# Kernel tuning notes

Hardware: AMD Instinct MI355X
Metric: run time of the kernel (lower is better)

## Reference

```python
import jax, jax.numpy as jnp
import numpy as np

B, S, N, E = 4, 256, 257, 256  # batch, seq_len, num_nodes (=S+1), num_edges (=S)
IN, OUT, EDIM = 128, 128, 16


def setup_inputs() -> dict:
    key = jax.random.key(0)
    k = jax.random.split(key, 7)
    x = jax.random.normal(k[0], (B, S, N, IN), jnp.float32)
    ei = jax.random.randint(k[1], (B, S, E, 2), 0, N)
    drop = jax.random.uniform(k[2], (B, S, E, 2)) < 0.05
    edge_index = jnp.where(drop, -1, ei)
    edge_attr = jax.random.normal(k[3], (B, S, E, EDIM), jnp.float32)
    node_mask = jnp.ones((B, S, N), dtype=bool)  # accepted but unused by forward
    edge_mask = jax.random.uniform(k[4], (B, S, E)) > 0.1
    W = jax.random.normal(k[5], (IN, OUT), jnp.float32) * (1.0 / np.sqrt(IN))
    a = jax.random.normal(k[6], (2 * OUT + EDIM, 1), jnp.float32) * 0.05
    return {"x": x, "edge_index": edge_index, "edge_attr": edge_attr,
            "node_mask": node_mask, "edge_mask": edge_mask, "W": W, "a": a}


def reference(x, edge_index, edge_attr, node_mask, edge_mask, W, a):
    # x: [B,S,N,IN] -> h: [B,S,N,D]
    h = x @ W
    Bq, Sq = h.shape[0], h.shape[1]
    src_idx = edge_index[..., 0]  # [B,S,E]
    tgt_idx = edge_index[..., 1]

    def gather(idx):  # [B,S,E] -> [B,S,E,D], gather node features along node dim
        return jnp.take_along_axis(h, jnp.clip(idx, 0, None)[..., None], axis=2)

    # src/tgt features, zeroed where index < 0 (invalid edge endpoint)
    src = jnp.where((src_idx >= 0)[..., None], gather(src_idx), 0.0)
    tgt = jnp.where((tgt_idx >= 0)[..., None], gather(tgt_idx), 0.0)

    # attention logits over concatenated [src | tgt | edge_attr]
    cat = jnp.concatenate([src, tgt, edge_attr], axis=-1)  # [B,S,E,2D+edim]
    e = jax.nn.leaky_relu((cat @ a)[..., 0], negative_slope=0.2)  # [B,S,E]
    e = jnp.where(edge_mask, e, -jnp.inf)
    # rows with no finite entry are zeroed (-> uniform softmax), as in torch code
    all_invalid = ~jnp.isfinite(e).any(axis=-1, keepdims=True)
    e = jnp.where(all_invalid, 0.0, e)
    alpha = jax.nn.softmax(e, axis=-1)  # [B,S,E]

    # masked edges get index 0 (they still contribute alpha-weighted feats to node 0,
    # matching the original scatter semantics)
    vsrc = jnp.where(edge_mask, src_idx, 0)
    vtgt = jnp.where(edge_mask, tgt_idx, 0)
    x_src = jnp.take_along_axis(h, vsrc[..., None], axis=2) * alpha[..., None]
    x_tgt = jnp.take_along_axis(h, vtgt[..., None], axis=2) * alpha[..., None]

    # scatter-add over edges into node buffer (equivalent to the torch 5D
    # scatter_ + sum over the edge dim, without materializing [B,S,E,N,D])
    bi = jnp.arange(Bq)[:, None, None]
    si = jnp.arange(Sq)[None, :, None]
    agg = (jnp.zeros(h.shape, h.dtype)
           .at[bi, si, vtgt].add(x_src)
           .at[bi, si, vsrc].add(x_tgt))
    return jax.nn.elu(agg)
```

## Files before the change

### kernel.cpp

```cpp
#include <hip/hip_runtime.h>
#include <cfloat>
#include <cmath>


#define BB 4
#define SS 256
#define NNODE 257
#define EE 256
#define DIN 128
#define DOUT 128
#define EDIMC 16
#define NMASK (BB * SS * EE)

#define WS_FLAG_OFF  0
#define WS_MASK_OFF  1024
#define WS_ALPHA_OFF 266240

__global__ void detect_mask_kernel(const unsigned int* __restrict__ m, int* flag) {
    unsigned int v = 0;
    for (int i = threadIdx.x; i < 256; i += 64) v |= m[i];
    int bad = (v > 1u) ? 1 : 0;
    bad = __any(bad) ? 1 : 0;
    if (threadIdx.x == 0) *flag = bad;
}

__global__ __launch_bounds__(256) void mask_canon_kernel(
        const int* __restrict__ m32, const unsigned char* __restrict__ m8,
        const int* __restrict__ flag, unsigned char* __restrict__ out) {
    const bool byteLayout = (*flag != 0);
    int i = blockIdx.x * 256 + threadIdx.x;
    if (i < NMASK) out[i] = byteLayout ? (m8[i] != 0) : (m32[i] != 0);
}

__global__ __launch_bounds__(256) void gemm_kernel(const float* __restrict__ x,
                                                   const float* __restrict__ W,
                                                   float* __restrict__ h) {
    __shared__ float xs[32][132];
    __shared__ float wsh[32][132];
    const int tid = threadIdx.x;
    const long m0 = (long)blockIdx.x * 128;
    const int tm = tid >> 4;
    const int tn = tid & 15;
    const int mr = tm * 8, nr = tn * 8;
    float acc[8][8];
#pragma unroll
    for (int i = 0; i < 8; ++i)
#pragma unroll
        for (int j = 0; j < 8; ++j) acc[i][j] = 0.f;

    for (int kt = 0; kt < 4; ++kt) {
#pragma unroll
        for (int j = 0; j < 4; ++j) {
            int idx = j * 256 + tid;
            int row = idx >> 3;
            int kq  = idx & 7;
            float4 v = *reinterpret_cast<const float4*>(
                x + (m0 + row) * DIN + kt * 32 + kq * 4);
            xs[kq * 4 + 0][row] = v.x;
            xs[kq * 4 + 1][row] = v.y;
            xs[kq * 4 + 2][row] = v.z;
            xs[kq * 4 + 3][row] = v.w;
        }
#pragma unroll
        for (int j = 0; j < 4; ++j) {
            int idx = j * 256 + tid;
            int row = idx >> 5;
            int nq  = idx & 31;
            float4 v = *reinterpret_cast<const float4*>(
                W + (kt * 32 + row) * DOUT + nq * 4);
            *reinterpret_cast<float4*>(&wsh[row][nq * 4]) = v;
        }
        __syncthreads();
#pragma unroll
        for (int k = 0; k < 32; ++k) {
            float4 a0 = *reinterpret_cast<const float4*>(&xs[k][mr]);
            float4 a1 = *reinterpret_cast<const float4*>(&xs[k][mr + 4]);
            float4 b0 = *reinterpret_cast<const float4*>(&wsh[k][nr]);
            float4 b1 = *reinterpret_cast<const float4*>(&wsh[k][nr + 4]);
            float av[8] = {a0.x, a0.y, a0.z, a0.w, a1.x, a1.y, a1.z, a1.w};
            float bv[8] = {b0.x, b0.y, b0.z, b0.w, b1.x, b1.y, b1.z, b1.w};
#pragma unroll
            for (int i = 0; i < 8; ++i)
#pragma unroll
                for (int jj = 0; jj < 8; ++jj)
                    acc[i][jj] = fmaf(av[i], bv[jj], acc[i][jj]);
        }
        __syncthreads();
    }
#pragma unroll
    for (int i = 0; i < 8; ++i) {
        float* dst = h + (m0 + mr + i) * DOUT + nr;
        *reinterpret_cast<float4*>(dst) =
            make_float4(acc[i][0], acc[i][1], acc[i][2], acc[i][3]);
        *reinterpret_cast<float4*>(dst + 4) =
            make_float4(acc[i][4], acc[i][5], acc[i][6], acc[i][7]);
    }
}

__global__ __launch_bounds__(256) void alpha_kernel(
        const float* __restrict__ h, const int* __restrict__ eidx,
        const float* __restrict__ eattr, const unsigned char* __restrict__ emask,
        const float* __restrict__ a, float* __restrict__ alpha_out) {
    __shared__ float pq[NNODE], pt[NNODE];
    __shared__ float ae[EDIMC];
    __shared__ float red[4];
    __shared__ int redi[4];
    const int tid = threadIdx.x;
    const int bs = blockIdx.x;
    const int lane = tid & 63, wave = tid >> 6;
    if (tid < EDIMC) ae[tid] = a[2 * DOUT + tid];
    const float a0 = a[lane], a1 = a[lane + 64];
    const float a2 = a[128 + lane], a3 = a[192 + lane];
    const float* hb = h + (long)bs * NNODE * DIN;
    for (int n = wave; n < NNODE; n += 4) {
        const float* hr = hb + n * DIN;
        float v0 = hr[lane], v1 = hr[lane + 64];
        float s = v0 * a0 + v1 * a1;
        float t = v0 * a2 + v1 * a3;
#pragma unroll
        for (int o = 32; o > 0; o >>= 1) {
            s += __shfl_xor(s, o);
            t += __shfl_xor(t, o);
        }
        if (lane == 0) { pq[n] = s; pt[n] = t; }
    }
    __syncthreads();

    const int e = tid;
    const long ebase = (long)bs * EE + e;
    const int si = eidx[2 * ebase];
    const int ti = eidx[2 * ebase + 1];
    const float4* ea4 = reinterpret_cast<const float4*>(eattr + ebase * EDIMC);
    float dea = 0.f;
#pragma unroll
    for (int j = 0; j < 4; ++j) {
        float4 u = ea4[j];
        dea += u.x * ae[4 * j] + u.y * ae[4 * j + 1] +
               u.z * ae[4 * j + 2] + u.w * ae[4 * j + 3];
    }
    float val = (si >= 0 ? pq[si] : 0.f) + (ti >= 0 ? pt[ti] : 0.f) + dea;
    val = val > 0.f ? val : 0.2f * val;
    const bool m = emask[ebase] != 0;

    float lg = m ? val : -FLT_MAX;
    float wm = lg;
    int anyv = m ? 1 : 0;
#pragma unroll
    for (int o = 32; o > 0; o >>= 1) {
        wm = fmaxf(wm, __shfl_xor(wm, o));
        anyv |= __shfl_xor(anyv, o);
    }
    if (lane == 0) { red[wave] = wm; redi[wave] = anyv; }
    __syncthreads();
    const float gmax = fmaxf(fmaxf(red[0], red[1]), fmaxf(red[2], red[3]));
    const int ganyv = redi[0] | redi[1] | redi[2] | redi[3];
    float ex = m ? expf(val - gmax) : 0.f;
    float sm = ex;
#pragma unroll
    for (int o = 32; o > 0; o >>= 1) sm += __shfl_xor(sm, o);
    __syncthreads();
    if (lane == 0) red[wave] = sm;
    __syncthreads();
    const float gsum = red[0] + red[1] + red[2] + red[3];
    alpha_out[ebase] = ganyv ? ex / gsum : (1.0f / EE);
}

__global__ __launch_bounds__(256) void agg_kernel(
        const float* __restrict__ h, const int* __restrict__ eidx,
        const unsigned char* __restrict__ emask, const float* __restrict__ alpha,
        float* __restrict__ out) {
    __shared__ float agg[NNODE * 32];
    const int tid = threadIdx.x;
    const int bs = blockIdx.x;
    const int dbase = blockIdx.y * 32;
    const int slot = tid >> 5, d = tid & 31;
    for (int i = tid; i < NNODE * 32; i += 256) agg[i] = 0.f;
    __syncthreads();

    const float* hb = h + (long)bs * NNODE * DIN + dbase;
    const long eb0 = (long)bs * EE;
    for (int e0 = 0; e0 < EE; e0 += 8) {
        const int e = e0 + slot;
        const float al = alpha[eb0 + e];
        if (al != 0.f) {
            const int si = eidx[2 * (eb0 + e)];
            const int ti = eidx[2 * (eb0 + e) + 1];
            const bool m = emask[eb0 + e] != 0;
            int vs = m ? si : 0; if (vs < 0) vs += NNODE;
            int vt = m ? ti : 0; if (vt < 0) vt += NNODE;
            const float hs = hb[(long)vs * DIN + d];
            const float ht = hb[(long)vt * DIN + d];
            atomicAdd(&agg[vt * 32 + d], al * hs);
            atomicAdd(&agg[vs * 32 + d], al * ht);
        }
    }
    __syncthreads();

    float* ob = out + (long)bs * NNODE * DIN + dbase;
    for (int n = slot; n < NNODE; n += 8) {
        const float v = agg[n * 32 + d];
        ob[(long)n * DIN + d] = v > 0.f ? v : expm1f(v);
    }
}

extern "C" void kernel_launch(void* const* d_in, const int* in_sizes, int n_in,
                              void* d_out, int out_size, void* d_ws, size_t ws_size,
                              hipStream_t stream) {
    const float* x     = (const float*)d_in[0];
    const int* eidx    = (const int*)d_in[1];
    const float* eattr = (const float*)d_in[2];
    const void* emraw  = d_in[4];
    const float* W     = (const float*)d_in[5];
    const float* a     = (const float*)d_in[6];
    float* out = (float*)d_out;

    char* ws = (char*)d_ws;
    int* flag            = (int*)(ws + WS_FLAG_OFF);
    unsigned char* mask8 = (unsigned char*)(ws + WS_MASK_OFF);
    float* alpha         = (float*)(ws + WS_ALPHA_OFF);
    float* h             = out;

    detect_mask_kernel<<<1, 64, 0, stream>>>((const unsigned int*)emraw, flag);
    mask_canon_kernel<<<NMASK / 256, 256, 0, stream>>>(
        (const int*)emraw, (const unsigned char*)emraw, flag, mask8);

    const int M_BLOCKS = (BB * SS * NNODE) / 128;
    gemm_kernel<<<M_BLOCKS, 256, 0, stream>>>(x, W, h);
    alpha_kernel<<<BB * SS, 256, 0, stream>>>(h, eidx, eattr, mask8, a, alpha);
    agg_kernel<<<dim3(BB * SS, 4), 256, 0, stream>>>(h, eidx, mask8, alpha, out);
}
```

Before: 647.4 us.

## Fuse attention projections into GEMM epilogue and stage h slices in LDS for aggregation

The GEMM epilogue now computes the per-node dot products with the src and tgt halves of the attention vector, reducing across the 16 column threads with shuffles and writing pq/pt to workspace. A lighter alpha kernel then reads only those scalars instead of re-reading all of h. The aggregation kernel now splits the feature dimension into 16-wide slices, stages each slice of h and the edge metadata in shared memory, and accumulates with padded LDS atomics. This removes a full re-read of h and the scattered global gathers. In exchange it launches twice as many agg blocks, uses more LDS per block, and needs a larger workspace, falling back to the old path when the workspace is too small.

```diff
diff --git a/kernel.cpp b/kernel.cpp
--- a/kernel.cpp
+++ b/kernel.cpp
@@ -11,10 +11,14 @@
 #define DOUT 128
 #define EDIMC 16
 #define NMASK (BB * SS * EE)
+#define MROWS (BB * SS * NNODE)
 
 #define WS_FLAG_OFF  0
 #define WS_MASK_OFF  1024
 #define WS_ALPHA_OFF 266240
+#define WS_PQ_OFF    (WS_ALPHA_OFF + NMASK * 4)
+#define WS_PT_OFF    (WS_PQ_OFF + MROWS * 4)
+#define WS_NEEDED    (WS_PT_OFF + MROWS * 4)
 
 __global__ void detect_mask_kernel(const unsigned int* __restrict__ m, int* flag) {
     unsigned int v = 0;
@@ -34,7 +38,10 @@
 
 __global__ __launch_bounds__(256) void gemm_kernel(const float* __restrict__ x,
                                                    const float* __restrict__ W,
-                                                   float* __restrict__ h) {
+                                                   const float* __restrict__ a,
+                                                   float* __restrict__ h,
+                                                   float* __restrict__ pq,
+                                                   float* __restrict__ pt) {
     __shared__ float xs[32][132];
     __shared__ float wsh[32][132];
     const int tid = threadIdx.x;
@@ -95,6 +102,86 @@
         *reinterpret_cast<float4*>(dst + 4) =
             make_float4(acc[i][4], acc[i][5], acc[i][6], acc[i][7]);
     }
+
+    if (pq != nullptr) {
+        float aq[8], at_[8];
+#pragma unroll
+        for (int j = 0; j < 8; ++j) {
+            aq[j]  = a[nr + j];
+            at_[j] = a[DOUT + nr + j];
+        }
+#pragma unroll
+        for (int i = 0; i < 8; ++i) {
+            float s = 0.f, t = 0.f;
+#pragma unroll
+            for (int j = 0; j < 8; ++j) {
+                s = fmaf(acc[i][j], aq[j], s);
+                t = fmaf(acc[i][j], at_[j], t);
+            }
+#pragma unroll
+            for (int o = 1; o < 16; o <<= 1) {
+                s += __shfl_xor(s, o);
+                t += __shfl_xor(t, o);
+            }
+            if (tn == 0) {
+                pq[m0 + mr + i] = s;
+                pt[m0 + mr + i] = t;
+            }
+        }
+    }
+}
+
+__global__ __launch_bounds__(256) void alpha2_kernel(
+        const float* __restrict__ pq, const float* __restrict__ pt,
+        const int* __restrict__ eidx, const float* __restrict__ eattr,
+        const unsigned char* __restrict__ emask, const float* __restrict__ a,
+        float* __restrict__ alpha_out) {
+    __shared__ float ae[EDIMC];
+    __shared__ float red[4];
+    __shared__ int redi[4];
+    const int tid = threadIdx.x;
+    const int bs = blockIdx.x;
+    const int lane = tid & 63, wave = tid >> 6;
+    if (tid < EDIMC) ae[tid] = a[2 * DOUT + tid];
+    __syncthreads();
+
+    const long ebase = (long)bs * EE + tid;
+    const int si = eidx[2 * ebase];
+    const int ti = eidx[2 * ebase + 1];
+    const float4* ea4 = reinterpret_cast<const float4*>(eattr + ebase * EDIMC);
+    float dea = 0.f;
+#pragma unroll
+    for (int j = 0; j < 4; ++j) {
+        float4 u = ea4[j];
+        dea += u.x * ae[4 * j] + u.y * ae[4 * j + 1] +
+               u.z * ae[4 * j + 2] + u.w * ae[4 * j + 3];
+    }
+    const long nb = (long)bs * NNODE;
+    float val = (si >= 0 ? pq[nb + si] : 0.f) + (ti >= 0 ? pt[nb + ti] : 0.f) + dea;
+    val = val > 0.f ? val : 0.2f * val;
+    const bool m = emask[ebase] != 0;
+
+    float lg = m ? val : -FLT_MAX;
+    float wm = lg;
+    int anyv = m ? 1 : 0;
+#pragma unroll
+    for (int o = 32; o > 0; o >>= 1) {
+        wm = fmaxf(wm, __shfl_xor(wm, o));
+        anyv |= __shfl_xor(anyv, o);
+    }
+    if (lane == 0) { red[wave] = wm; redi[wave] = anyv; }
+    __syncthreads();
+    const float gmax = fmaxf(fmaxf(red[0], red[1]), fmaxf(red[2], red[3]));
+    const int ganyv = redi[0] | redi[1] | redi[2] | redi[3];
+    float ex = m ? expf(val - gmax) : 0.f;
+    float sm = ex;
+#pragma unroll
+    for (int o = 32; o > 0; o >>= 1) sm += __shfl_xor(sm, o);
+    __syncthreads();
+    if (lane == 0) red[wave] = sm;
+    __syncthreads();
+    const float gsum = red[0] + red[1] + red[2] + red[3];
+    alpha_out[ebase] = ganyv ? ex / gsum : (1.0f / EE);
 }
 
 __global__ __launch_bounds__(256) void alpha_kernel(
@@ -126,8 +213,7 @@
     }
     __syncthreads();
 
-    const int e = tid;
-    const long ebase = (long)bs * EE + e;
+    const long ebase = (long)bs * EE + tid;
     const int si = eidx[2 * ebase];
     const int ti = eidx[2 * ebase + 1];
     const float4* ea4 = reinterpret_cast<const float4*>(eattr + ebase * EDIMC);
@@ -165,40 +251,60 @@
     alpha_out[ebase] = ganyv ? ex / gsum : (1.0f / EE);
 }
 
+#define DSL 16
+#define PAD 17
 __global__ __launch_bounds__(256) void agg_kernel(
         const float* __restrict__ h, const int* __restrict__ eidx,
         const unsigned char* __restrict__ emask, const float* __restrict__ alpha,
         float* __restrict__ out) {
-    __shared__ float agg[NNODE * 32];
+    __shared__ float hs[NNODE * PAD];
+    __shared__ float acc[NNODE * PAD];
+    __shared__ float meta_a[EE];
+    __shared__ int   meta_v[EE];
     const int tid = threadIdx.x;
     const int bs = blockIdx.x;
-    const int dbase = blockIdx.y * 32;
-    const int slot = tid >> 5, d = tid & 31;
-    for (int i = tid; i < NNODE * 32; i += 256) agg[i] = 0.f;
-    __syncthreads();
+    const int dbase = blockIdx.y * DSL;
+    const int slot = tid >> 4, d = tid & 15;
 
     const float* hb = h + (long)bs * NNODE * DIN + dbase;
-    const long eb0 = (long)bs * EE;
-    for (int e0 = 0; e0 < EE; e0 += 8) {
+
+    for (int i = tid; i < NNODE * 4; i += 256) {
+        int row = i >> 2, q = i & 3;
+        float4 v = *reinterpret_cast<const float4*>(hb + (long)row * DIN + q * 4);
+        float* dst = &hs[row * PAD + q * 4];
+        dst[0] = v.x; dst[1] = v.y; dst[2] = v.z; dst[3] = v.w;
+    }
+    for (int i = tid; i < NNODE * PAD; i += 256) acc[i] = 0.f;
+    {
+        const long eb = (long)bs * EE + tid;
+        const int si = eidx[2 * eb];
+        const int ti = eidx[2 * eb + 1];
+        const bool m = emask[eb] != 0;
+        int vs = m ? si : 0; if (vs < 0) vs += NNODE;
+        int vt = m ? ti : 0; if (vt < 0) vt += NNODE;
+        meta_a[tid] = alpha[eb];
+        meta_v[tid] = vs | (vt << 16);
+    }
+    __syncthreads();
+
+#pragma unroll 4
+    for (int e0 = 0; e0 < EE; e0 += 16) {
         const int e = e0 + slot;
-        const float al = alpha[eb0 + e];
+        const float al = meta_a[e];
         if (al != 0.f) {
-            const int si = eidx[2 * (eb0 + e)];
-            const int ti = eidx[2 * (eb0 + e) + 1];
-            const bool m = emask[eb0 + e] != 0;
-            int vs = m ? si : 0; if (vs < 0) vs += NNODE;
-            int vt = m ? ti : 0; if (vt < 0) vt += NNODE;
-            const float hs = hb[(long)vs * DIN + d];
-            const float ht = hb[(long)vt * DIN + d];
-            atomicAdd(&agg[vt * 32 + d], al * hs);
-            atomicAdd(&agg[vs * 32 + d], al * ht);
+            const int pv = meta_v[e];
+            const int vs = pv & 0xffff, vt = pv >> 16;
+            const float hsv = hs[vs * PAD + d];
+            const float htv = hs[vt * PAD + d];
+            atomicAdd(&acc[vt * PAD + d], al * hsv);
+            atomicAdd(&acc[vs * PAD + d], al * htv);
         }
     }
     __syncthreads();
 
     float* ob = out + (long)bs * NNODE * DIN + dbase;
-    for (int n = slot; n < NNODE; n += 8) {
-        const float v = agg[n * 32 + d];
+    for (int n = slot; n < NNODE; n += 16) {
+        const float v = acc[n * PAD + d];
         ob[(long)n * DIN + d] = v > 0.f ? v : expm1f(v);
     }
 }
@@ -219,13 +325,20 @@
     unsigned char* mask8 = (unsigned char*)(ws + WS_MASK_OFF);
     float* alpha         = (float*)(ws + WS_ALPHA_OFF);
     float* h             = out;
+    const bool fused     = (ws_size >= (size_t)WS_NEEDED);
+    float* pq            = fused ? (float*)(ws + WS_PQ_OFF) : nullptr;
+    float* pt            = fused ? (float*)(ws + WS_PT_OFF) : nullptr;
 
     detect_mask_kernel<<<1, 64, 0, stream>>>((const unsigned int*)emraw, flag);
     mask_canon_kernel<<<NMASK / 256, 256, 0, stream>>>(
         (const int*)emraw, (const unsigned char*)emraw, flag, mask8);
 
-    const int M_BLOCKS = (BB * SS * NNODE) / 128;
-    gemm_kernel<<<M_BLOCKS, 256, 0, stream>>>(x, W, h);
-    alpha_kernel<<<BB * SS, 256, 0, stream>>>(h, eidx, eattr, mask8, a, alpha);
-    agg_kernel<<<dim3(BB * SS, 4), 256, 0, stream>>>(h, eidx, mask8, alpha, out);
-}
+    const int M_BLOCKS = MROWS / 128;
+    gemm_kernel<<<M_BLOCKS, 256, 0, stream>>>(x, W, a, h, pq, pt);
+    if (fused) {
+        alpha2_kernel<<<BB * SS, 256, 0, stream>>>(pq, pt, eidx, eattr, mask8, a, alpha);
+    } else {
+        alpha_kernel<<<BB * SS, 256, 0, stream>>>(h, eidx, eattr, mask8, a, alpha);
+    }
+    agg_kernel<<<dim3(BB * SS, 8), 256, 0, stream>>>(h, eidx, mask8, alpha, out);
+}
```

Result: faster. 626.9 us (-3.2%).
